# Performance work log

Hardware: AMD Instinct MI355X
Metric: run time of the kernel (lower is better)

Reference implementation:

```python
import jax, jax.numpy as jnp
import numpy as np

D_MODEL = 96
D_INNER = 192   # ssm_ratio * d_model
R = 6           # dt_rank = ceil(96/16)
DH = 32         # d_inner // dt_rank (per-head dim)
K = 4           # scan directions
N = 16          # d_state
EPS = 1e-5


def setup_inputs() -> dict:
    key = jax.random.key(0)
    ks = jax.random.split(key, 10)
    B, H, W = 8, 64, 64
    f = lambda k, s, sc: jax.random.normal(k, s, jnp.float32) * sc
    return dict(
        x=jax.random.normal(ks[0], (B, H, W, D_MODEL), jnp.float32),
        w_in=f(ks[1], (D_MODEL, D_INNER), 0.02),
        w_conv=f(ks[2], (3, 3, 1, D_INNER), 0.1),      # depthwise HWIO
        b_conv=f(ks[3], (D_INNER,), 0.1),
        x_proj_weight=f(ks[4], (K, R + 2 * N, D_INNER), 0.02),
        A_logs=f(ks[5], (K, R), 0.5),
        Ds=jnp.ones((K, R, DH), jnp.float32),
        dt_bias=0.1 * jax.random.uniform(ks[6], (K, R), jnp.float32),
        ln_g=jnp.ones((D_INNER,), jnp.float32),
        ln_b=jnp.zeros((D_INNER,), jnp.float32),
        w_out=f(ks[7], (D_INNER, D_MODEL), 0.02),
    )


def _cross_scan(x):
    # x: (B,H,W,C) -> (B,L,4,C): [row-major, col-major, rev row, rev col]
    B, H, W, C = x.shape
    x0 = x.reshape(B, H * W, C)
    x1 = jnp.transpose(x, (0, 2, 1, 3)).reshape(B, H * W, C)
    return jnp.stack([x0, x1, x0[:, ::-1], x1[:, ::-1]], axis=2)


def _cross_merge(ys, H, W):
    # ys: (B,L,4,C) -> (B,L,C) summed after undoing each scan order
    B, L, _, C = ys.shape
    y_row = ys[:, :, 0] + ys[:, :, 2][:, ::-1]
    y_col = ys[:, :, 1] + ys[:, :, 3][:, ::-1]
    y_col = jnp.transpose(y_col.reshape(B, W, H, C), (0, 2, 1, 3)).reshape(B, L, C)
    return y_row + y_col


def _selective_scan(us, dts, As, Bs, Cs, Dsr, dtb):
    # us:(B,L,KR,DH) dts:(B,L,KR) As:(KR,) Bs,Cs:(B,L,K,N) Dsr:(KR,DH) dtb:(KR,)
    dt = jax.nn.softplus(dts + dtb)                 # (B,L,KR)
    decay = jnp.exp(dt * As)                        # (B,L,KR)
    xu = dt[..., None] * us                         # (B,L,KR,DH)
    Bh = jnp.repeat(Bs, R, axis=2)                  # (B,L,KR,N) head h -> group h//R
    Ch = jnp.repeat(Cs, R, axis=2)
    B_, L, KR, _ = us.shape
    tfirst = lambda a: jnp.moveaxis(a, 1, 0)

    def step(h, inp):
        dec, xu_t, b_t, c_t = inp                   # (B,KR),(B,KR,DH),(B,KR,N),(B,KR,N)
        h = dec[:, :, None, None] * h + xu_t[..., None] * b_t[:, :, None, :]
        y = jnp.einsum('bkdn,bkn->bkd', h, c_t)
        return h, y

    h0 = jnp.zeros((B_, KR, DH, N), us.dtype)
    _, ys = jax.lax.scan(step, h0, (tfirst(decay), tfirst(xu), tfirst(Bh), tfirst(Ch)))
    ys = jnp.moveaxis(ys, 0, 1)                     # (B,L,KR,DH)
    return ys + us * Dsr                            # skip term D*u


def reference(x, w_in, w_conv, b_conv, x_proj_weight, A_logs, Ds, dt_bias, ln_g, ln_b, w_out):
    B, H, W, _ = x.shape
    L = H * W
    xi = x @ w_in                                   # in_proj (no bias)
    xi = jax.lax.conv_general_dilated(
        xi, w_conv, (1, 1), 'SAME', feature_group_count=D_INNER,
        dimension_numbers=('NHWC', 'HWIO', 'NHWC')) + b_conv
    xi = jax.nn.silu(xi)
    xs = _cross_scan(xi)                            # (B,L,4,D_INNER)
    x_dbl = jnp.einsum('blkd,kcd->blkc', xs, x_proj_weight)
    dts = x_dbl[..., :R].reshape(B, L, K * R)
    Bs = x_dbl[..., R:R + N]                        # (B,L,K,N)
    Cs = x_dbl[..., R + N:]
    us = xs.reshape(B, L, K * R, DH)
    As = -jnp.exp(A_logs.astype(jnp.float32)).reshape(K * R)
    Dsr = Ds.reshape(K * R, DH)
    dtb = dt_bias.reshape(K * R)
    ys = _selective_scan(us, dts, As, Bs, Cs, Dsr, dtb)   # (B,L,KR,DH)
    y = _cross_merge(ys.reshape(B, L, K, R * DH), H, W)   # (B,L,D_INNER)
    mu = y.mean(-1, keepdims=True)
    var = ((y - mu) ** 2).mean(-1, keepdims=True)
    y = (y - mu) / jnp.sqrt(var + EPS) * ln_g + ln_b
    y = y.reshape(B, H, W, D_INNER)
    return y @ w_out                                # out_proj (no bias)
```

## Files before the change

### kernel.cpp

```cpp
#include <hip/hip_runtime.h>
#include <hip/hip_bf16.h>

#define BB 8
#define LL 4096
#define DM 96
#define DI 192
#define RRR 6
#define DHH 32
#define KKK 4
#define NNN 16
#define KRR 24
#define NCH 64
#define TT 64
#define RST 48

__device__ __forceinline__ float softplus_f(float x){
    float ax = fabsf(x);
    return fmaxf(x, 0.f) + __logf(1.f + __expf(-ax));
}
__device__ __forceinline__ float silu_f(float x){ return x / (1.f + __expf(-x)); }

__global__ void k0p(const float* __restrict__ W, const float* __restrict__ g,
                    const float* __restrict__ bta, const float* __restrict__ w_out,
                    float* __restrict__ WpR, float* __restrict__ wg, float* __restrict__ sgbw){
    int i = blockIdx.x * 256 + threadIdx.x;
    if (i < DI * 160){
        int d = i / 160, cc = i % 160; int gq = cc / 40, nc = cc % 40;
        int dir = (gq == 0) ? 0 : (gq == 1) ? 2 : (gq == 2) ? 1 : 3;
        float v = 0.f;
        if (nc < 6) v = W[(dir * 38 + nc) * DI + d];
        else if (nc >= 8) v = W[(dir * 38 + (nc - 2)) * DI + d];
        WpR[i] = v;
    } else if (i < DI * 160 + DI * DM){
        int j = i - DI * 160; int c = j / DM;
        wg[j] = w_out[j] * g[c];
    } else if (i < DI * 160 + DI * DM + DM){
        int m = i - (DI * 160 + DI * DM);
        float s = 0.f, t = 0.f;
        for (int c = 0; c < DI; ++c){
            float w = w_out[c * DM + m];
            s = fmaf(g[c], w, s);
            t = fmaf(bta[c], w, t);
        }
        sgbw[m] = s; sgbw[DM + m] = t;
    }
}

__global__ __launch_bounds__(384) void k1_inproj(const float* __restrict__ x,
                                                 const float* __restrict__ w_in,
                                                 float* __restrict__ xw){
    __shared__ float xT[DM][36];
    int pix0 = blockIdx.x * 32;
    for (int i = threadIdx.x; i < 32 * 24; i += 384){
        int c4 = i % 24, p = i / 24;
        float4 v = *(const float4*)(x + (size_t)(pix0 + p) * DM + c4 * 4);
        xT[c4 * 4 + 0][p] = v.x; xT[c4 * 4 + 1][p] = v.y;
        xT[c4 * 4 + 2][p] = v.z; xT[c4 * 4 + 3][p] = v.w;
    }
    __syncthreads();
    int cg = threadIdx.x % 48, pg = threadIdx.x / 48;
    int p0 = pg * 4;
    float4 acc[4];
    #pragma unroll
    for (int i = 0; i < 4; ++i) acc[i] = make_float4(0.f, 0.f, 0.f, 0.f);
    const float* wcol = w_in + cg * 4;
    for (int d = 0; d < DM; ++d){
        float4 w4 = *(const float4*)(wcol + d * DI);
        float4 xa = *(const float4*)(&xT[d][p0]);
        float xs[4] = {xa.x, xa.y, xa.z, xa.w};
        #pragma unroll
        for (int pi = 0; pi < 4; ++pi){
            acc[pi].x = fmaf(xs[pi], w4.x, acc[pi].x);
            acc[pi].y = fmaf(xs[pi], w4.y, acc[pi].y);
            acc[pi].z = fmaf(xs[pi], w4.z, acc[pi].z);
            acc[pi].w = fmaf(xs[pi], w4.w, acc[pi].w);
        }
    }
    #pragma unroll
    for (int pi = 0; pi < 4; ++pi)
        *(float4*)(xw + (size_t)(pix0 + p0 + pi) * DI + cg * 4) = acc[pi];
}

__global__ void k2_conv(const float* __restrict__ xw, const float* __restrict__ wc,
                        const float* __restrict__ bc, float* __restrict__ xi,
                        float* __restrict__ xiT){
    int gid = blockIdx.x * 256 + threadIdx.x;
    int c4 = gid % 48; int pix = gid / 48;
    int b = pix >> 12; int l = pix & 4095; int h = l >> 6; int w = l & 63;
    int c = c4 * 4;
    float4 acc = *(const float4*)(bc + c);
    #pragma unroll
    for (int dh = 0; dh < 3; ++dh){
        int hh = h + dh - 1; if ((unsigned)hh >= 64u) continue;
        #pragma unroll
        for (int dw = 0; dw < 3; ++dw){
            int ww2 = w + dw - 1; if ((unsigned)ww2 >= 64u) continue;
            float4 tap = *(const float4*)(xw + (size_t)((b << 12) + (hh << 6) + ww2) * DI + c);
            float4 wv  = *(const float4*)(wc + (dh * 3 + dw) * DI + c);
            acc.x = fmaf(tap.x, wv.x, acc.x);
            acc.y = fmaf(tap.y, wv.y, acc.y);
            acc.z = fmaf(tap.z, wv.z, acc.z);
            acc.w = fmaf(tap.w, wv.w, acc.w);
        }
    }
    acc.x = silu_f(acc.x); acc.y = silu_f(acc.y); acc.z = silu_f(acc.z); acc.w = silu_f(acc.w);
    *(float4*)(xi + (size_t)pix * DI + c) = acc;
    int lT = ((l & 63) << 6) | (l >> 6);
    *(float4*)(xiT + (size_t)((b << 12) + lT) * DI + c) = acc;
}

__global__ __launch_bounds__(320) void k3seq(const float* __restrict__ xi,
                                             const float* __restrict__ WpR,
                                             const float* __restrict__ A_logs,
                                             const float* __restrict__ dtb,
                                             float* __restrict__ rec){
    __shared__ float xT[96][36];
    int b = blockIdx.y;
    int l0 = blockIdx.x * 32;
    const float* src = xi + ((((size_t)b) << 12) + l0) * DI;
    int kg = threadIdx.x % 40, pg = threadIdx.x / 40;
    int p0 = pg * 4;
    float4 acc[4];
    #pragma unroll
    for (int i = 0; i < 4; ++i) acc[i] = make_float4(0.f, 0.f, 0.f, 0.f);
    const float* wcol = WpR + kg * 4;
    #pragma unroll
    for (int half = 0; half < 2; ++half){
        __syncthreads();
        for (int i = threadIdx.x; i < 32 * 24; i += 320){
            int c4 = i % 24, p = i / 24;
            float4 v = *(const float4*)(src + (size_t)p * DI + half * 96 + c4 * 4);
            xT[c4 * 4 + 0][p] = v.x; xT[c4 * 4 + 1][p] = v.y;
            xT[c4 * 4 + 2][p] = v.z; xT[c4 * 4 + 3][p] = v.w;
        }
        __syncthreads();
        const float* w = wcol + half * 96 * 160;
        for (int d = 0; d < 96; ++d){
            float4 w4 = *(const float4*)(w + d * 160);
            float4 xa = *(const float4*)(&xT[d][p0]);
            float xs[4] = {xa.x, xa.y, xa.z, xa.w};
            #pragma unroll
            for (int pi = 0; pi < 4; ++pi){
                acc[pi].x = fmaf(xs[pi], w4.x, acc[pi].x);
                acc[pi].y = fmaf(xs[pi], w4.y, acc[pi].y);
                acc[pi].z = fmaf(xs[pi], w4.z, acc[pi].z);
                acc[pi].w = fmaf(xs[pi], w4.w, acc[pi].w);
            }
        }
    }
    int gq = kg / 10;
    int dir = (gq == 0) ? 0 : (gq == 1) ? 2 : (gq == 2) ? 1 : 3;
    int nc0 = (kg % 10) * 4;
    float* rb = rec + (size_t)(b * KKK + dir) * LL * RST;
    float A0 = 0.f, A1 = 0.f, A2 = 0.f, A3 = 0.f, b0 = 0.f, b1 = 0.f, b2 = 0.f, b3 = 0.f;
    if (nc0 == 0){
        A0 = -__expf(A_logs[dir * RRR + 0]); b0 = dtb[dir * RRR + 0];
        A1 = -__expf(A_logs[dir * RRR + 1]); b1 = dtb[dir * RRR + 1];
        A2 = -__expf(A_logs[dir * RRR + 2]); b2 = dtb[dir * RRR + 2];
        A3 = -__expf(A_logs[dir * RRR + 3]); b3 = dtb[dir * RRR + 3];
    } else if (nc0 == 4){
        A0 = -__expf(A_logs[dir * RRR + 4]); b0 = dtb[dir * RRR + 4];
        A1 = -__expf(A_logs[dir * RRR + 5]); b1 = dtb[dir * RRR + 5];
    }
    #pragma unroll
    for (int pi = 0; pi < 4; ++pi){
        int l = l0 + p0 + pi;
        int lT = ((l & 63) << 6) | (l >> 6);
        int t;
        if (dir == 0) t = l;
        else if (dir == 2) t = LL - 1 - l;
        else if (dir == 1) t = lT;
        else t = LL - 1 - lT;
        float* rw = rb + (size_t)t * RST;
        float4 v = acc[pi];
        if (nc0 == 0){
            float4 dt4, dc4;
            dt4.x = softplus_f(v.x + b0); dc4.x = __expf(dt4.x * A0);
            dt4.y = softplus_f(v.y + b1); dc4.y = __expf(dt4.y * A1);
            dt4.z = softplus_f(v.z + b2); dc4.z = __expf(dt4.z * A2);
            dt4.w = softplus_f(v.w + b3); dc4.w = __expf(dt4.w * A3);
            *(float4*)(rw + 0) = dt4;
            *(float4*)(rw + 8) = dc4;
        } else if (nc0 == 4){
            float4 dt4, dc4;
            dt4.x = softplus_f(v.x + b0); dc4.x = __expf(dt4.x * A0);
            dt4.y = softplus_f(v.y + b1); dc4.y = __expf(dt4.y * A1);
            dt4.z = 0.f; dt4.w = 0.f; dc4.z = 0.f; dc4.w = 0.f;
            *(float4*)(rw + 4)  = dt4;
            *(float4*)(rw + 12) = dc4;
        } else {
            *(float4*)(rw + nc0 + 8) = v;
        }
    }
}

__global__ __launch_bounds__(192) void k4a(const float* __restrict__ xi, const float* __restrict__ xiT,
                                           const float* __restrict__ rec,
                                           float* __restrict__ Pb, float* __restrict__ Sb){
    int chunk = blockIdx.x, k = blockIdx.y, b = blockIdx.z;
    int r = threadIdx.x >> 5, d = threadIdx.x & 31;
    int kr = k * RRR + r;
    const float* rp = rec + ((size_t)(b * KKK + k) * LL + chunk * TT) * RST;
    const float* xb = ((k & 1) ? xiT : xi) + (((size_t)b) << 12) * DI + r * DHH + d;
    const float* up; ptrdiff_t ust;
    if (k < 2){ up = xb + (size_t)(chunk * TT) * DI;          ust = DI;  }
    else      { up = xb + (size_t)(LL - 1 - chunk * TT) * DI; ust = -(ptrdiff_t)DI; }
    float h[NNN];
    #pragma unroll
    for (int n = 0; n < NNN; ++n) h[n] = 0.f;
    float P = 1.f;
    #pragma unroll 4
    for (int tt = 0; tt < TT; ++tt){
        float dt  = rp[r];
        float dec = rp[8 + r];
        float u = *up;
        float xu = dt * u;
        P *= dec;
        float Bv[NNN];
        *(float4*)(Bv + 0)  = *(const float4*)(rp + 16);
        *(float4*)(Bv + 4)  = *(const float4*)(rp + 20);
        *(float4*)(Bv + 8)  = *(const float4*)(rp + 24);
        *(float4*)(Bv + 12) = *(const float4*)(rp + 28);
        #pragma unroll
        for (int n = 0; n < NNN; ++n) h[n] = fmaf(dec, h[n], xu * Bv[n]);
        rp += RST; up += ust;
    }
    size_t sb = (((size_t)(b * KRR + kr) * NCH + chunk) * DHH + d) * NNN;
    #pragma unroll
    for (int n = 0; n < NNN; ++n) Sb[sb + n] = h[n];
    if (d == 0) Pb[(size_t)(b * KRR + kr) * NCH + chunk] = P;
}

__global__ __launch_bounds__(256) void k4b(const float* __restrict__ Pb, float* __restrict__ Sb){
    int scan = blockIdx.x >> 1;
    int half = blockIdx.x & 1;
    int tid = half * 256 + threadIdx.x;
    size_t base = (size_t)scan * NCH * 512 + tid;
    const float* Pp = Pb + (size_t)scan * NCH;
    float s[NCH];
    #pragma unroll
    for (int c = 0; c < NCH; ++c) s[c] = Sb[base + (size_t)c * 512];
    float hb = 0.f;
    #pragma unroll
    for (int c = 0; c < NCH; ++c){
        float nv = fmaf(Pp[c], hb, s[c]);
        Sb[base + (size_t)c * 512] = hb;
        hb = nv;
    }
}

__global__ __launch_bounds__(192) void k4c(const float* __restrict__ xi, const float* __restrict__ xiT,
                                           const float* __restrict__ rec,
                                           const float* __restrict__ Ds, const float* __restrict__ Sb,
                                           __hip_bfloat16* __restrict__ ybuf){
    int chunk = blockIdx.x, k = blockIdx.y, b = blockIdx.z;
    int r = threadIdx.x >> 5, d = threadIdx.x & 31;
    int kr = k * RRR + r;
    float Dv = Ds[kr * DHH + d];
    float h[NNN];
    size_t sb = (((size_t)(b * KRR + kr) * NCH + chunk) * DHH + d) * NNN;
    #pragma unroll
    for (int n = 0; n < NNN; ++n) h[n] = Sb[sb + n];
    const float* rp = rec + ((size_t)(b * KKK + k) * LL + chunk * TT) * RST;
    const float* xb = ((k & 1) ? xiT : xi) + (((size_t)b) << 12) * DI + r * DHH + d;
    const float* up; ptrdiff_t ust;
    if (k < 2){ up = xb + (size_t)(chunk * TT) * DI;          ust = DI;  }
    else      { up = xb + (size_t)(LL - 1 - chunk * TT) * DI; ust = -(ptrdiff_t)DI; }
    __hip_bfloat16* yp = ybuf + ((size_t)(k * BB + b) * LL + chunk * TT) * DI + r * DHH + d;
    #pragma unroll 2
    for (int tt = 0; tt < TT; ++tt){
        float dt  = rp[r];
        float dec = rp[8 + r];
        float u = *up;
        float xu = dt * u;
        float Bv[NNN], Cv[NNN];
        *(float4*)(Bv + 0)  = *(const float4*)(rp + 16);
        *(float4*)(Bv + 4)  = *(const float4*)(rp + 20);
        *(float4*)(Bv + 8)  = *(const float4*)(rp + 24);
        *(float4*)(Bv + 12) = *(const float4*)(rp + 28);
        *(float4*)(Cv + 0)  = *(const float4*)(rp + 32);
        *(float4*)(Cv + 4)  = *(const float4*)(rp + 36);
        *(float4*)(Cv + 8)  = *(const float4*)(rp + 40);
        *(float4*)(Cv + 12) = *(const float4*)(rp + 44);
        float y = 0.f;
        #pragma unroll
        for (int n = 0; n < NNN; ++n){
            h[n] = fmaf(dec, h[n], xu * Bv[n]);
            y = fmaf(h[n], Cv[n], y);
        }
        y = fmaf(u, Dv, y);
        *yp = __float2bfloat16(y);
        rp += RST; up += ust; yp += DI;
    }
}

__global__ __launch_bounds__(256) void k5_out(const __hip_bfloat16* __restrict__ ybuf,
                       const float* __restrict__ wg, const float* __restrict__ sgbw,
                       float* __restrict__ out){
    __shared__ float yT[DI][36];
    __shared__ float rsL[32], rmL[32];
    int pix0 = blockIdx.x * 32;
    int b = pix0 >> 12;
    int l0 = pix0 & 4095;
    const __hip_bfloat16* y0 = ybuf + (size_t)(0 * BB + b) * LL * DI;
    const __hip_bfloat16* y1 = ybuf + (size_t)(1 * BB + b) * LL * DI;
    const __hip_bfloat16* y2 = ybuf + (size_t)(2 * BB + b) * LL * DI;
    const __hip_bfloat16* y3 = ybuf + (size_t)(3 * BB + b) * LL * DI;
    for (int i = threadIdx.x; i < 32 * DI; i += 256){
        int c = i % DI, p = i / DI;
        int l = l0 + p; int hh = l >> 6, ww = l & 63;
        int lT = (ww << 6) | hh;
        float s = __bfloat162float(y0[(size_t)l * DI + c])
                + __bfloat162float(y2[(size_t)(LL - 1 - l) * DI + c])
                + __bfloat162float(y1[(size_t)lT * DI + c])
                + __bfloat162float(y3[(size_t)(LL - 1 - lT) * DI + c]);
        yT[c][p] = s;
    }
    __syncthreads();
    {
        int p = threadIdx.x >> 3, cg = threadIdx.x & 7;
        float s = 0.f, s2 = 0.f;
        for (int c = cg; c < DI; c += 8){ float v = yT[c][p]; s += v; s2 = fmaf(v, v, s2); }
        s += __shfl_xor(s, 1, 64); s2 += __shfl_xor(s2, 1, 64);
        s += __shfl_xor(s, 2, 64); s2 += __shfl_xor(s2, 2, 64);
        s += __shfl_xor(s, 4, 64); s2 += __shfl_xor(s2, 4, 64);
        if (cg == 0){
            float mu = s * (1.f / DI);
            float var = s2 * (1.f / DI) - mu * mu;
            float rs = rsqrtf(var + 1e-5f);
            rsL[p] = rs; rmL[p] = rs * mu;
        }
    }
    __syncthreads();
    if (threadIdx.x < 192){
        int mg = threadIdx.x % 24, pg = threadIdx.x / 24;
        int p0 = pg * 4;
        float4 acc[4];
        #pragma unroll
        for (int i = 0; i < 4; ++i) acc[i] = make_float4(0.f, 0.f, 0.f, 0.f);
        const float* wcol = wg + mg * 4;
        for (int c = 0; c < DI; ++c){
            float4 w4 = *(const float4*)(wcol + c * DM);
            float4 yv = *(const float4*)(&yT[c][p0]);
            float ys[4] = {yv.x, yv.y, yv.z, yv.w};
            #pragma unroll
            for (int pi = 0; pi < 4; ++pi){
                acc[pi].x = fmaf(ys[pi], w4.x, acc[pi].x);
                acc[pi].y = fmaf(ys[pi], w4.y, acc[pi].y);
                acc[pi].z = fmaf(ys[pi], w4.z, acc[pi].z);
                acc[pi].w = fmaf(ys[pi], w4.w, acc[pi].w);
            }
        }
        float4 sg4 = *(const float4*)(sgbw + mg * 4);
        float4 bw4 = *(const float4*)(sgbw + DM + mg * 4);
        #pragma unroll
        for (int pi = 0; pi < 4; ++pi){
            float rs = rsL[p0 + pi], rm = rmL[p0 + pi];
            float4 o;
            o.x = fmaf(acc[pi].x, rs, fmaf(-rm, sg4.x, bw4.x));
            o.y = fmaf(acc[pi].y, rs, fmaf(-rm, sg4.y, bw4.y));
            o.z = fmaf(acc[pi].z, rs, fmaf(-rm, sg4.z, bw4.z));
            o.w = fmaf(acc[pi].w, rs, fmaf(-rm, sg4.w, bw4.w));
            *(float4*)(out + (size_t)(pix0 + p0 + pi) * DM + mg * 4) = o;
        }
    }
}

extern "C" void kernel_launch(void* const* d_in, const int* in_sizes, int n_in,
                              void* d_out, int out_size, void* d_ws, size_t ws_size,
                              hipStream_t stream){
    const float* x      = (const float*)d_in[0];
    const float* w_in   = (const float*)d_in[1];
    const float* w_conv = (const float*)d_in[2];
    const float* b_conv = (const float*)d_in[3];
    const float* xproj  = (const float*)d_in[4];
    const float* A_logs = (const float*)d_in[5];
    const float* Ds     = (const float*)d_in[6];
    const float* dtbias = (const float*)d_in[7];
    const float* ln_g   = (const float*)d_in[8];
    const float* ln_b   = (const float*)d_in[9];
    const float* w_out  = (const float*)d_in[10];
    float* out = (float*)d_out;

    float* ws   = (float*)d_ws;
    float* xi   = ws;
    float* xiT  = xi + 6291456;
    float* Sb   = xiT + 6291456;
    float* Pb   = Sb + 6291456;
    float* WpR  = Pb + 16384;
    float* wg   = WpR + 30720;
    float* sgbw = wg + 18432;
    float* big  = sgbw + 192;
    float* xw   = big;
    float* rec  = big;
    __hip_bfloat16* ybuf = (__hip_bfloat16*)(big + 6291456);

    k0p<<<193, 256, 0, stream>>>(xproj, ln_g, ln_b, w_out, WpR, wg, sgbw);
    k1_inproj<<<1024, 384, 0, stream>>>(x, w_in, xw);
    k2_conv<<<6144, 256, 0, stream>>>(xw, w_conv, b_conv, xi, xiT);
    k3seq<<<dim3(128, BB), 320, 0, stream>>>(xi, WpR, A_logs, dtbias, rec);
    k4a<<<dim3(NCH, KKK, BB), 192, 0, stream>>>(xi, xiT, rec, Pb, Sb);
    k4b<<<384, 256, 0, stream>>>(Pb, Sb);
    k4c<<<dim3(NCH, KKK, BB), 192, 0, stream>>>(xi, xiT, rec, Ds, Sb, ybuf);
    k5_out<<<1024, 256, 0, stream>>>(ybuf, wg, sgbw, out);
}
```

Before: 289.3 us.

## Split x_proj by scan direction reading transposed input; unroll GEMM inner loops

The x_proj kernel now gets a grid axis for the direction pair. Row-major directions read xi and column-major directions read the transposed xiT, so the rec writes become contiguous or reversed-contiguous instead of scattered by a transposed index. Each block handles 64 pixels and 80 output columns. The in_proj, x_proj and out_proj inner loops are also unrolled by 8 with batched loads to expose memory-level parallelism, at the cost of more registers.

```diff
diff --git a/kernel.cpp b/kernel.cpp
--- a/kernel.cpp
+++ b/kernel.cpp
@@ -64,16 +64,23 @@
     #pragma unroll
     for (int i = 0; i < 4; ++i) acc[i] = make_float4(0.f, 0.f, 0.f, 0.f);
     const float* wcol = w_in + cg * 4;
-    for (int d = 0; d < DM; ++d){
-        float4 w4 = *(const float4*)(wcol + d * DI);
-        float4 xa = *(const float4*)(&xT[d][p0]);
-        float xs[4] = {xa.x, xa.y, xa.z, xa.w};
-        #pragma unroll
-        for (int pi = 0; pi < 4; ++pi){
-            acc[pi].x = fmaf(xs[pi], w4.x, acc[pi].x);
-            acc[pi].y = fmaf(xs[pi], w4.y, acc[pi].y);
-            acc[pi].z = fmaf(xs[pi], w4.z, acc[pi].z);
-            acc[pi].w = fmaf(xs[pi], w4.w, acc[pi].w);
+    for (int d0 = 0; d0 < DM; d0 += 8){
+        float4 wv[8], xv[8];
+        #pragma unroll
+        for (int j = 0; j < 8; ++j){
+            wv[j] = *(const float4*)(wcol + (d0 + j) * DI);
+            xv[j] = *(const float4*)(&xT[d0 + j][p0]);
+        }
+        #pragma unroll
+        for (int j = 0; j < 8; ++j){
+            float xs[4] = {xv[j].x, xv[j].y, xv[j].z, xv[j].w};
+            #pragma unroll
+            for (int pi = 0; pi < 4; ++pi){
+                acc[pi].x = fmaf(xs[pi], wv[j].x, acc[pi].x);
+                acc[pi].y = fmaf(xs[pi], wv[j].y, acc[pi].y);
+                acc[pi].z = fmaf(xs[pi], wv[j].z, acc[pi].z);
+                acc[pi].w = fmaf(xs[pi], wv[j].w, acc[pi].w);
+            }
         }
     }
     #pragma unroll
@@ -110,46 +117,54 @@
 }
 
 __global__ __launch_bounds__(320) void k3seq(const float* __restrict__ xi,
+                                             const float* __restrict__ xiT,
                                              const float* __restrict__ WpR,
                                              const float* __restrict__ A_logs,
                                              const float* __restrict__ dtb,
                                              float* __restrict__ rec){
-    __shared__ float xT[96][36];
-    int b = blockIdx.y;
-    int l0 = blockIdx.x * 32;
-    const float* src = xi + ((((size_t)b) << 12) + l0) * DI;
-    int kg = threadIdx.x % 40, pg = threadIdx.x / 40;
+    __shared__ float xT[96][68];
+    int z = blockIdx.y, b = blockIdx.z;
+    int l0 = blockIdx.x * 64;
+    const float* src = (z ? xiT : xi) + ((((size_t)b) << 12) + l0) * DI;
+    int kg = threadIdx.x % 20, pg = threadIdx.x / 20;
     int p0 = pg * 4;
     float4 acc[4];
     #pragma unroll
     for (int i = 0; i < 4; ++i) acc[i] = make_float4(0.f, 0.f, 0.f, 0.f);
-    const float* wcol = WpR + kg * 4;
+    const float* wcol = WpR + z * 80 + kg * 4;
     #pragma unroll
     for (int half = 0; half < 2; ++half){
         __syncthreads();
-        for (int i = threadIdx.x; i < 32 * 24; i += 320){
+        for (int i = threadIdx.x; i < 64 * 24; i += 320){
             int c4 = i % 24, p = i / 24;
             float4 v = *(const float4*)(src + (size_t)p * DI + half * 96 + c4 * 4);
             xT[c4 * 4 + 0][p] = v.x; xT[c4 * 4 + 1][p] = v.y;
             xT[c4 * 4 + 2][p] = v.z; xT[c4 * 4 + 3][p] = v.w;
         }
         __syncthreads();
-        const float* w = wcol + half * 96 * 160;
-        for (int d = 0; d < 96; ++d){
-            float4 w4 = *(const float4*)(w + d * 160);
-            float4 xa = *(const float4*)(&xT[d][p0]);
-            float xs[4] = {xa.x, xa.y, xa.z, xa.w};
+        const float* wp = wcol + half * 96 * 160;
+        for (int d0 = 0; d0 < 96; d0 += 8){
+            float4 wv[8], xv[8];
             #pragma unroll
-            for (int pi = 0; pi < 4; ++pi){
-                acc[pi].x = fmaf(xs[pi], w4.x, acc[pi].x);
-                acc[pi].y = fmaf(xs[pi], w4.y, acc[pi].y);
-                acc[pi].z = fmaf(xs[pi], w4.z, acc[pi].z);
-                acc[pi].w = fmaf(xs[pi], w4.w, acc[pi].w);
+            for (int j = 0; j < 8; ++j){
+                wv[j] = *(const float4*)(wp + (d0 + j) * 160);
+                xv[j] = *(const float4*)(&xT[d0 + j][p0]);
             }
-        }
-    }
-    int gq = kg / 10;
-    int dir = (gq == 0) ? 0 : (gq == 1) ? 2 : (gq == 2) ? 1 : 3;
+            #pragma unroll
+            for (int j = 0; j < 8; ++j){
+                float xs[4] = {xv[j].x, xv[j].y, xv[j].z, xv[j].w};
+                #pragma unroll
+                for (int pi = 0; pi < 4; ++pi){
+                    acc[pi].x = fmaf(xs[pi], wv[j].x, acc[pi].x);
+                    acc[pi].y = fmaf(xs[pi], wv[j].y, acc[pi].y);
+                    acc[pi].z = fmaf(xs[pi], wv[j].z, acc[pi].z);
+                    acc[pi].w = fmaf(xs[pi], wv[j].w, acc[pi].w);
+                }
+            }
+        }
+    }
+    int sub = kg / 10;
+    int dir = (z == 0) ? (sub == 0 ? 0 : 2) : (sub == 0 ? 1 : 3);
     int nc0 = (kg % 10) * 4;
     float* rb = rec + (size_t)(b * KKK + dir) * LL * RST;
     float A0 = 0.f, A1 = 0.f, A2 = 0.f, A3 = 0.f, b0 = 0.f, b1 = 0.f, b2 = 0.f, b3 = 0.f;
@@ -165,12 +180,7 @@
     #pragma unroll
     for (int pi = 0; pi < 4; ++pi){
         int l = l0 + p0 + pi;
-        int lT = ((l & 63) << 6) | (l >> 6);
-        int t;
-        if (dir == 0) t = l;
-        else if (dir == 2) t = LL - 1 - l;
-        else if (dir == 1) t = lT;
-        else t = LL - 1 - lT;
+        int t = (sub == 0) ? l : (LL - 1 - l);
         float* rw = rb + (size_t)t * RST;
         float4 v = acc[pi];
         if (nc0 == 0){
@@ -339,16 +349,23 @@
         #pragma unroll
         for (int i = 0; i < 4; ++i) acc[i] = make_float4(0.f, 0.f, 0.f, 0.f);
         const float* wcol = wg + mg * 4;
-        for (int c = 0; c < DI; ++c){
-            float4 w4 = *(const float4*)(wcol + c * DM);
-            float4 yv = *(const float4*)(&yT[c][p0]);
-            float ys[4] = {yv.x, yv.y, yv.z, yv.w};
+        for (int c0 = 0; c0 < DI; c0 += 8){
+            float4 wv[8], yv[8];
             #pragma unroll
-            for (int pi = 0; pi < 4; ++pi){
-                acc[pi].x = fmaf(ys[pi], w4.x, acc[pi].x);
-                acc[pi].y = fmaf(ys[pi], w4.y, acc[pi].y);
-                acc[pi].z = fmaf(ys[pi], w4.z, acc[pi].z);
-                acc[pi].w = fmaf(ys[pi], w4.w, acc[pi].w);
+            for (int j = 0; j < 8; ++j){
+                wv[j] = *(const float4*)(wcol + (c0 + j) * DM);
+                yv[j] = *(const float4*)(&yT[c0 + j][p0]);
+            }
+            #pragma unroll
+            for (int j = 0; j < 8; ++j){
+                float ys[4] = {yv[j].x, yv[j].y, yv[j].z, yv[j].w};
+                #pragma unroll
+                for (int pi = 0; pi < 4; ++pi){
+                    acc[pi].x = fmaf(ys[pi], wv[j].x, acc[pi].x);
+                    acc[pi].y = fmaf(ys[pi], wv[j].y, acc[pi].y);
+                    acc[pi].z = fmaf(ys[pi], wv[j].z, acc[pi].z);
+                    acc[pi].w = fmaf(ys[pi], wv[j].w, acc[pi].w);
+                }
             }
         }
         float4 sg4 = *(const float4*)(sgbw + mg * 4);
@@ -398,7 +415,7 @@
     k0p<<<193, 256, 0, stream>>>(xproj, ln_g, ln_b, w_out, WpR, wg, sgbw);
     k1_inproj<<<1024, 384, 0, stream>>>(x, w_in, xw);
     k2_conv<<<6144, 256, 0, stream>>>(xw, w_conv, b_conv, xi, xiT);
-    k3seq<<<dim3(128, BB), 320, 0, stream>>>(xi, WpR, A_logs, dtbias, rec);
+    k3seq<<<dim3(64, 2, BB), 320, 0, stream>>>(xi, xiT, WpR, A_logs, dtbias, rec);
     k4a<<<dim3(NCH, KKK, BB), 192, 0, stream>>>(xi, xiT, rec, Pb, Sb);
     k4b<<<384, 256, 0, stream>>>(Pb, Sb);
     k4c<<<dim3(NCH, KKK, BB), 192, 0, stream>>>(xi, xiT, rec, Ds, Sb, ybuf);
```

After: 283.7 us. No clear change (-1.9%).
